# Optimization experiments

Hardware: AMD Instinct MI355X
Metric: run time of the kernel (lower is better)

## Reference

```python
import jax, jax.numpy as jnp
import numpy as np

B, PP, LP, H = 128, 1024, 128, 256  # graphs, protein atoms/graph, ligand atoms/graph, hidden
NP, NL = B * PP, B * LP


def setup_inputs() -> dict:
    key = jax.random.key(0)
    ks = jax.random.split(key, 16)
    s = 0.02
    return {
        "protein_pos": 10.0 * jax.random.normal(ks[0], (NP, 3), jnp.float32),
        "ligand_pos": 10.0 * jax.random.normal(ks[1], (NL, 3), jnp.float32),
        "protein_element": jax.random.randint(ks[2], (NP,), 0, 128),
        "protein_aa": jax.random.randint(ks[3], (NP,), 0, 32),
        "protein_is_backbone": jax.random.randint(ks[4], (NP,), 0, 2),
        "ligand_type": jax.random.randint(ks[5], (NL,), 0, 16),
        "protein_batch": jnp.repeat(jnp.arange(B), PP),  # block-contiguous segments
        "ligand_batch": jnp.repeat(jnp.arange(B), LP),
        "E_elem": s * jax.random.normal(ks[6], (128, H), jnp.float32),
        "E_aa": s * jax.random.normal(ks[7], (32, H), jnp.float32),
        "E_bb": s * jax.random.normal(ks[8], (2, H), jnp.float32),
        "E_lig": s * jax.random.normal(ks[9], (16, H), jnp.float32),
        "Wd1": s * jax.random.normal(ks[10], (H, H), jnp.float32),
        "bd1": jnp.zeros((H,), jnp.float32),
        "Wd2": s * jax.random.normal(ks[11], (H, H), jnp.float32),
        "bd2": jnp.zeros((H,), jnp.float32),
        "Wa1": s * jax.random.normal(ks[12], (2 * H + 2, H), jnp.float32),
        "ba1": jnp.zeros((H,), jnp.float32),
        "Wa2": s * jax.random.normal(ks[13], (H, 1), jnp.float32),
        "ba2": jnp.zeros((1,), jnp.float32),
    }


def _pool_by_batch(x, batch, bsz):
    # mean-pool rows of x into bsz segments (index_add_ + bincount in torch)
    summed = jax.ops.segment_sum(x, batch, num_segments=bsz)
    counts = jax.ops.segment_sum(jnp.ones((x.shape[0],), x.dtype), batch, num_segments=bsz)
    return summed / jnp.maximum(counts, 1.0)[:, None]


def reference(protein_pos, ligand_pos, protein_element, protein_aa, protein_is_backbone,
              ligand_type, protein_batch, ligand_batch,
              E_elem, E_aa, E_bb, E_lig, Wd1, bd1, Wd2, bd2, Wa1, ba1, Wa2, ba2):
    # protein / ligand node embeddings
    h_protein = E_elem[protein_element] + E_aa[protein_aa] + E_bb[protein_is_backbone]
    h_ligand = E_lig[ligand_type]

    # compose_context: protein first, then ligand (mask_ligand = [0]*NP + [1]*NL)
    h_ctx = jnp.concatenate([h_protein, h_ligand], axis=0)

    # stub denoiser: pointwise 2-layer SiLU MLP producing out['h']
    h_out = jax.nn.silu(h_ctx @ Wd1 + bd1) @ Wd2 + bd2
    protein_h = h_out[:protein_pos.shape[0]]
    ligand_h = h_out[protein_pos.shape[0]:]

    pooled_protein = _pool_by_batch(protein_h, protein_batch, B)  # [B, H]
    pooled_ligand = _pool_by_batch(ligand_h, ligand_batch, B)     # [B, H]

    # contact features: per-graph cdist(lig, prot), min over protein atoms,
    # then mean & min over ligand atoms. Uniform block layout -> dense reshape.
    prot = protein_pos.reshape(B, PP, 3)
    lig = ligand_pos.reshape(B, LP, 3)
    d2 = jnp.sum((lig[:, :, None, :] - prot[:, None, :, :]) ** 2, axis=-1)  # [B, LP, PP]
    dist = jnp.sqrt(d2)
    min_lp = dist.min(axis=2)                                    # [B, LP]
    contact = jnp.stack([min_lp.mean(axis=1), min_lp.min(axis=1)], axis=-1)  # [B, 2]

    graph_feat = jnp.concatenate([pooled_protein, pooled_ligand, contact], axis=-1)  # [B, 2H+2]
    affinity = (jax.nn.silu(graph_feat @ Wa1 + ba1) @ Wa2 + ba2).squeeze(-1)  # [B]
    return affinity
```

## Files before the change

### kernel.cpp

```cpp
#include <hip/hip_runtime.h>
#include <hip/hip_bf16.h>

typedef _Float16 f16;
typedef _Float16 h4 __attribute__((ext_vector_type(4)));

#define B_   128
#define PP_  1024
#define LP_  128
#define H_   256


__global__ void __launch_bounds__(256) prep_k(
    const float* __restrict__ W1,
    const float* __restrict__ Ee, const float* __restrict__ Ea,
    const float* __restrict__ Eb, const float* __restrict__ El,
    const float* __restrict__ bd1,
    const float* __restrict__ ppos, const float* __restrict__ lpos,
    f16* __restrict__ tbl, float* __restrict__ cbuf, float* __restrict__ ysum)
{
  __shared__ float px[4 * 264], py[4 * 264], pz[4 * 264];
  __shared__ float lmin[128];
  __shared__ float src[256];
  const int bid = blockIdx.x, tid = threadIdx.x;
  if (bid < 256) ysum[bid * 256 + tid] = 0.f;

  if (bid < 178) {
    const float* s;
    float badd = 0.f;
    if (bid < 128)      s = Ee + bid * 256;
    else if (bid < 160) s = Ea + (bid - 128) * 256;
    else if (bid < 162) { s = Eb + (bid - 160) * 256; badd = bd1[tid]; }
    else                { s = El + (bid - 162) * 256; badd = bd1[tid]; }
    src[tid] = s[tid];
    __syncthreads();
    float a0 = 0.f, a1 = 0.f, a2 = 0.f, a3 = 0.f;
#pragma unroll 4
    for (int k = 0; k < 256; k += 4) {
      a0 += src[k]     * W1[(k)     * 256 + tid];
      a1 += src[k + 1] * W1[(k + 1) * 256 + tid];
      a2 += src[k + 2] * W1[(k + 2) * 256 + tid];
      a3 += src[k + 3] * W1[(k + 3) * 256 + tid];
    }
    tbl[bid * 256 + tid] = (f16)(((a0 + a1) + (a2 + a3)) + badd);
    return;
  }

  const int b = bid - 178;
#pragma unroll
  for (int r = 0; r < 4; ++r) {
    const int i = r * 256 + tid;
    const int d = (i >> 8) * 264 + (i & 255);
    const float* p = ppos + ((size_t)b * PP_ + i) * 3;
    px[d] = p[0]; py[d] = p[1]; pz[d] = p[2];
  }
  __syncthreads();
  {
    const int lig = tid >> 1, prt = tid & 1;
    const float* lp = lpos + ((size_t)b * LP_ + lig) * 3;
    const float lx = lp[0], ly = lp[1], lz = lp[2];
    float m = 3.4e38f;
#pragma unroll 1
    for (int s2 = prt * 2; s2 < prt * 2 + 2; ++s2) {
      const float4* X4 = (const float4*)(px + s2 * 264);
      const float4* Y4 = (const float4*)(py + s2 * 264);
      const float4* Z4 = (const float4*)(pz + s2 * 264);
#pragma unroll 4
      for (int i = 0; i < 64; ++i) {
        float4 X = X4[i], Y = Y4[i], Z = Z4[i];
        float dx, dy, dz, d2;
        dx = lx - X.x; dy = ly - Y.x; dz = lz - Z.x;
        d2 = dx * dx + dy * dy + dz * dz; m = fminf(m, d2);
        dx = lx - X.y; dy = ly - Y.y; dz = lz - Z.y;
        d2 = dx * dx + dy * dy + dz * dz; m = fminf(m, d2);
        dx = lx - X.z; dy = ly - Y.z; dz = lz - Z.z;
        d2 = dx * dx + dy * dy + dz * dz; m = fminf(m, d2);
        dx = lx - X.w; dy = ly - Y.w; dz = lz - Z.w;
        d2 = dx * dx + dy * dy + dz * dz; m = fminf(m, d2);
      }
    }
    m = fminf(m, __shfl_xor(m, 1));
    if (prt == 0) lmin[lig] = sqrtf(m);
  }
  __syncthreads();
  if (tid < 64) {
    const float a0 = lmin[tid], a1 = lmin[tid + 64];
    float sm = a0 + a1, mn = fminf(a0, a1);
#pragma unroll
    for (int off = 32; off; off >>= 1) {
      sm += __shfl_down(sm, off);
      mn = fminf(mn, __shfl_down(mn, off));
    }
    if (tid == 0) {
      cbuf[b * 2 + 0] = sm * (1.f / (float)LP_);
      cbuf[b * 2 + 1] = mn;
    }
  }
}

__global__ void __launch_bounds__(256, 4) gpool_k(
    const int* __restrict__ pel, const int* __restrict__ paa,
    const int* __restrict__ pbb, const int* __restrict__ ltyp,
    const f16* __restrict__ tbl, float* __restrict__ ysum)
{
  const int tid = threadIdx.x;
  const int wave = __builtin_amdgcn_readfirstlane(tid >> 6);
  const int lane = tid & 63;
  const int batch = blockIdx.x / 9, g = blockIdx.x % 9;
  const int c0 = lane * 4;
  float acc[4] = {0.f, 0.f, 0.f, 0.f};

  if (g < 8) {
    const int base = batch * PP_ + g * 128 + wave * 32;
#pragma unroll
    for (int ch = 0; ch < 4; ++ch) {
      const int cb = base + ch * 8;
      const int4 e0 = *(const int4*)(pel + cb), e1 = *(const int4*)(pel + cb + 4);
      const int4 a0 = *(const int4*)(paa + cb), a1 = *(const int4*)(paa + cb + 4);
      const int4 b0 = *(const int4*)(pbb + cb), b1 = *(const int4*)(pbb + cb + 4);
      const int el[8] = {e0.x, e0.y, e0.z, e0.w, e1.x, e1.y, e1.z, e1.w};
      const int aa[8] = {a0.x, a0.y, a0.z, a0.w, a1.x, a1.y, a1.z, a1.w};
      const int bb[8] = {b0.x, b0.y, b0.z, b0.w, b1.x, b1.y, b1.z, b1.w};
      h4 s[8];
#pragma unroll
      for (int r = 0; r < 8; ++r) {
        h4 va = *(const h4*)(tbl + el[r] * 256 + c0);
        h4 vb = *(const h4*)(tbl + 32768 + aa[r] * 256 + c0);
        h4 vc = *(const h4*)(tbl + 40960 + bb[r] * 256 + c0);
        s[r] = (va + vb) + vc;
      }
#pragma unroll
      for (int r = 0; r < 8; ++r)
#pragma unroll
        for (int i = 0; i < 4; ++i) {
          float pre = (float)s[r][i];
          acc[i] += pre * __builtin_amdgcn_rcpf(1.f + __expf(-pre));
        }
    }
    float* pool = ysum + batch * 256 + c0;
#pragma unroll
    for (int i = 0; i < 4; ++i) atomicAdd(pool + i, acc[i]);
  } else {
    const int base = batch * LP_ + wave * 32;
#pragma unroll
    for (int ch = 0; ch < 4; ++ch) {
      const int cb = base + ch * 8;
      const int4 l0 = *(const int4*)(ltyp + cb), l1 = *(const int4*)(ltyp + cb + 4);
      const int lt[8] = {l0.x, l0.y, l0.z, l0.w, l1.x, l1.y, l1.z, l1.w};
      h4 s[8];
#pragma unroll
      for (int r = 0; r < 8; ++r)
        s[r] = *(const h4*)(tbl + 41472 + lt[r] * 256 + c0);
#pragma unroll
      for (int r = 0; r < 8; ++r)
#pragma unroll
        for (int i = 0; i < 4; ++i) {
          float pre = (float)s[r][i];
          acc[i] += pre * __builtin_amdgcn_rcpf(1.f + __expf(-pre));
        }
    }
    float* pool = ysum + 32768 + batch * 256 + c0;
#pragma unroll
    for (int i = 0; i < 4; ++i) atomicAdd(pool + i, acc[i]);
  }
}

__global__ void __launch_bounds__(1024) head_k(
    const float* __restrict__ ysum, const float* __restrict__ cbuf,
    const float* __restrict__ W2, const float* __restrict__ bd2,
    const float* __restrict__ Wa1, const float* __restrict__ ba1,
    const float* __restrict__ Wa2, const float* __restrict__ ba2,
    float* __restrict__ out)
{
  __shared__ float ys[512], pooled[512], p2[1024], part[1024], red[4];
  const int b = blockIdx.x, tid = threadIdx.x;

  if (tid < 512)
    ys[tid] = (tid < 256) ? ysum[b * 256 + tid]
                          : ysum[32768 + b * 256 + (tid - 256)];
  __syncthreads();

  {
    const int kh2 = tid >> 9, h = (tid >> 8) & 1, n = tid & 255;
    const float* y = ys + h * 256 + kh2 * 128;
    const float* W = W2 + kh2 * 128 * 256 + n;
    float a[8];
#pragma unroll
    for (int u = 0; u < 8; ++u) a[u] = 0.f;
#pragma unroll 2
    for (int k = 0; k < 128; k += 8)
#pragma unroll
      for (int u = 0; u < 8; ++u)
        a[u] += y[k + u] * W[(k + u) * 256];
    p2[tid] = ((a[0] + a[1]) + (a[2] + a[3])) + ((a[4] + a[5]) + (a[6] + a[7]));
  }
  __syncthreads();
  if (tid < 512) {
    const int h = tid >> 8, n = tid & 255;
    const float scale = h ? (1.f / (float)LP_) : (1.f / (float)PP_);
    pooled[tid] = (p2[tid] + p2[512 + tid]) * scale + bd2[n];
  }
  __syncthreads();

  {
    const int kq = tid >> 8, j = tid & 255;
    const float* p = pooled + kq * 128;
    const float* W = Wa1 + kq * 128 * 256 + j;
    float a[8];
#pragma unroll
    for (int u = 0; u < 8; ++u) a[u] = 0.f;
#pragma unroll 2
    for (int n = 0; n < 128; n += 8)
#pragma unroll
      for (int u = 0; u < 8; ++u)
        a[u] += p[n + u] * W[(n + u) * 256];
    part[tid] = ((a[0] + a[1]) + (a[2] + a[3])) + ((a[4] + a[5]) + (a[6] + a[7]));
  }
  __syncthreads();

  if (tid < 256) {
    const float c0 = cbuf[b * 2], c1 = cbuf[b * 2 + 1];
    float pre = (part[tid] + part[256 + tid]) + (part[512 + tid] + part[768 + tid])
              + ba1[tid] + c0 * Wa1[512 * 256 + tid] + c1 * Wa1[513 * 256 + tid];
    float si = pre * __builtin_amdgcn_rcpf(1.f + __expf(-pre));
    float p = si * Wa2[tid];
#pragma unroll
    for (int off = 32; off; off >>= 1) p += __shfl_down(p, off);
    if ((tid & 63) == 0) red[tid >> 6] = p;
  }
  __syncthreads();
  if (tid == 0) out[b] = (red[0] + red[1]) + (red[2] + red[3]) + ba2[0];
}

extern "C" void kernel_launch(void* const* d_in, const int* in_sizes, int n_in,
                              void* d_out, int out_size, void* d_ws, size_t ws_size,
                              hipStream_t stream)
{
  const float* protein_pos = (const float*)d_in[0];
  const float* ligand_pos  = (const float*)d_in[1];
  const int*   pel  = (const int*)d_in[2];
  const int*   paa  = (const int*)d_in[3];
  const int*   pbb  = (const int*)d_in[4];
  const int*   ltyp = (const int*)d_in[5];
  const float* Ee  = (const float*)d_in[8];
  const float* Ea  = (const float*)d_in[9];
  const float* Eb  = (const float*)d_in[10];
  const float* El  = (const float*)d_in[11];
  const float* Wd1 = (const float*)d_in[12];
  const float* bd1 = (const float*)d_in[13];
  const float* Wd2 = (const float*)d_in[14];
  const float* bd2 = (const float*)d_in[15];
  const float* Wa1 = (const float*)d_in[16];
  const float* ba1 = (const float*)d_in[17];
  const float* Wa2 = (const float*)d_in[18];
  const float* ba2 = (const float*)d_in[19];
  float* out = (float*)d_out;

  char* ws = (char*)d_ws;
  f16*   tbl  = (f16*)(ws);
  float* cbuf = (float*)(ws + 98304);
  float* ysum = (float*)(ws + 102400);

  prep_k<<<306, 256, 0, stream>>>(Wd1, Ee, Ea, Eb, El, bd1,
                                  protein_pos, ligand_pos, tbl, cbuf, ysum);
  gpool_k<<<B_ * 9, 256, 0, stream>>>(pel, paa, pbb, ltyp, tbl, ysum);
  head_k<<<B_, 1024, 0, stream>>>(ysum, cbuf, Wd2, bd2, Wa1, ba1, Wa2, ba2, out);
}
```

Baseline: 141.3 us.

## Precompute SiLU over all element/aa/backbone combinations into a lookup table

Adds a kernel that evaluates SiLU(pre-activation) for every one of the 128*32*2 protein index combinations plus the 16 ligand types, and stores the results as an fp16 table. The pooling kernel then does a single gather per atom by combined index and only accumulates, with no per-atom exp or reciprocal. The aim is to replace 131k atoms' worth of transcendental math and three gathers each with 8208 table rows and one gather. In exchange it adds an extra kernel launch, about 4 MB of table writes, and a larger working set for random gathers, and it rounds the activation to fp16 before accumulation.

```diff
diff --git a/kernel.cpp b/kernel.cpp
--- a/kernel.cpp
+++ b/kernel.cpp
@@ -97,10 +97,26 @@
   }
 }
 
+__global__ void __launch_bounds__(256) combo_k(
+    const f16* __restrict__ tbl, f16* __restrict__ stbl)
+{
+  const int bid = blockIdx.x, tid = threadIdx.x;
+  float pre;
+  if (bid < 8192) {
+    const int el = bid >> 6, aa = (bid >> 1) & 31, bb = bid & 1;
+    pre = (float)tbl[el * 256 + tid]
+        + (float)tbl[32768 + aa * 256 + tid]
+        + (float)tbl[40960 + bb * 256 + tid];
+  } else {
+    pre = (float)tbl[41472 + (bid - 8192) * 256 + tid];
+  }
+  stbl[bid * 256 + tid] = (f16)(pre * __builtin_amdgcn_rcpf(1.f + __expf(-pre)));
+}
+
 __global__ void __launch_bounds__(256, 4) gpool_k(
     const int* __restrict__ pel, const int* __restrict__ paa,
     const int* __restrict__ pbb, const int* __restrict__ ltyp,
-    const f16* __restrict__ tbl, float* __restrict__ ysum)
+    const f16* __restrict__ stbl, float* __restrict__ ysum)
 {
   const int tid = threadIdx.x;
   const int wave = __builtin_amdgcn_readfirstlane(tid >> 6);
@@ -117,24 +133,20 @@
       const int4 e0 = *(const int4*)(pel + cb), e1 = *(const int4*)(pel + cb + 4);
       const int4 a0 = *(const int4*)(paa + cb), a1 = *(const int4*)(paa + cb + 4);
       const int4 b0 = *(const int4*)(pbb + cb), b1 = *(const int4*)(pbb + cb + 4);
-      const int el[8] = {e0.x, e0.y, e0.z, e0.w, e1.x, e1.y, e1.z, e1.w};
-      const int aa[8] = {a0.x, a0.y, a0.z, a0.w, a1.x, a1.y, a1.z, a1.w};
-      const int bb[8] = {b0.x, b0.y, b0.z, b0.w, b1.x, b1.y, b1.z, b1.w};
+      const int cmb[8] = {
+        e0.x * 64 + a0.x * 2 + b0.x, e0.y * 64 + a0.y * 2 + b0.y,
+        e0.z * 64 + a0.z * 2 + b0.z, e0.w * 64 + a0.w * 2 + b0.w,
+        e1.x * 64 + a1.x * 2 + b1.x, e1.y * 64 + a1.y * 2 + b1.y,
+        e1.z * 64 + a1.z * 2 + b1.z, e1.w * 64 + a1.w * 2 + b1.w };
       h4 s[8];
 #pragma unroll
-      for (int r = 0; r < 8; ++r) {
-        h4 va = *(const h4*)(tbl + el[r] * 256 + c0);
-        h4 vb = *(const h4*)(tbl + 32768 + aa[r] * 256 + c0);
-        h4 vc = *(const h4*)(tbl + 40960 + bb[r] * 256 + c0);
-        s[r] = (va + vb) + vc;
-      }
-#pragma unroll
-      for (int r = 0; r < 8; ++r)
-#pragma unroll
-        for (int i = 0; i < 4; ++i) {
-          float pre = (float)s[r][i];
-          acc[i] += pre * __builtin_amdgcn_rcpf(1.f + __expf(-pre));
-        }
+      for (int r = 0; r < 8; ++r)
+        s[r] = *(const h4*)(stbl + cmb[r] * 256 + c0);
+#pragma unroll
+      for (int r = 0; r < 8; ++r)
+#pragma unroll
+        for (int i = 0; i < 4; ++i)
+          acc[i] += (float)s[r][i];
     }
     float* pool = ysum + batch * 256 + c0;
 #pragma unroll
@@ -149,14 +161,12 @@
       h4 s[8];
 #pragma unroll
       for (int r = 0; r < 8; ++r)
-        s[r] = *(const h4*)(tbl + 41472 + lt[r] * 256 + c0);
-#pragma unroll
-      for (int r = 0; r < 8; ++r)
-#pragma unroll
-        for (int i = 0; i < 4; ++i) {
-          float pre = (float)s[r][i];
-          acc[i] += pre * __builtin_amdgcn_rcpf(1.f + __expf(-pre));
-        }
+        s[r] = *(const h4*)(stbl + (8192 + lt[r]) * 256 + c0);
+#pragma unroll
+      for (int r = 0; r < 8; ++r)
+#pragma unroll
+        for (int i = 0; i < 4; ++i)
+          acc[i] += (float)s[r][i];
     }
     float* pool = ysum + 32768 + batch * 256 + c0;
 #pragma unroll
@@ -259,9 +269,11 @@
   f16*   tbl  = (f16*)(ws);
   float* cbuf = (float*)(ws + 98304);
   float* ysum = (float*)(ws + 102400);
+  f16*   stbl = (f16*)(ws + 524288);
 
   prep_k<<<306, 256, 0, stream>>>(Wd1, Ee, Ea, Eb, El, bd1,
                                   protein_pos, ligand_pos, tbl, cbuf, ysum);
-  gpool_k<<<B_ * 9, 256, 0, stream>>>(pel, paa, pbb, ltyp, tbl, ysum);
+  combo_k<<<8208, 256, 0, stream>>>(tbl, stbl);
+  gpool_k<<<B_ * 9, 256, 0, stream>>>(pel, paa, pbb, ltyp, stbl, ysum);
   head_k<<<B_, 1024, 0, stream>>>(ysum, cbuf, Wd2, bd2, Wa1, ba1, Wa2, ba2, out);
 }
```

After: 143.9 us. Within noise of the previous version (+1.8%).
